# Kernel tuning notes

Hardware: AMD Instinct MI355X
Metric: run time of the kernel (lower is better)

The kernel has to match this reference:

```python
import jax, jax.numpy as jnp
import numpy as np

N_NODES = 50000


def _add_self_loops(src, dst, n):
    loop = jnp.arange(n, dtype=src.dtype)
    return jnp.concatenate([src, loop]), jnp.concatenate([dst, loop])


def gcn_conv(x, src, dst, W, b, n):
    # PyG GCNConv: out = D^-1/2 (A+I) D^-1/2 (x W) + b
    h = x @ W                                        # [N, out]
    deg = jnp.zeros((n,), h.dtype).at[dst].add(1.0)  # in-degree incl. self-loops
    dinv = jax.lax.rsqrt(jnp.maximum(deg, 1e-12))
    norm = dinv[src] * dinv[dst]                     # [E]
    msg = h[src] * norm[:, None]                     # [E, out] gather
    return jax.ops.segment_sum(msg, dst, num_segments=n) + b


def setup_inputs() -> dict:
    key = jax.random.key(0)
    ks = jax.random.split(key, 10)
    num_features, hidden = 256, 64
    x = jax.random.normal(ks[0], (N_NODES, num_features), jnp.float32)
    edge_index = jax.random.randint(ks[1], (2, 1600000), 0, N_NODES, jnp.int64)

    def glorot(k, fi, fo):
        s = jnp.sqrt(6.0 / (fi + fo)).astype(jnp.float32)
        return jax.random.uniform(k, (fi, fo), jnp.float32, -s, s)

    dims = [(num_features, 2 * hidden), (2 * hidden, hidden),
            (hidden, 2 * hidden), (2 * hidden, num_features)]
    params = {}
    for i, (fi, fo) in enumerate(dims):
        params[f"W{i+1}"] = glorot(ks[2 + i], fi, fo)
        params[f"b{i+1}"] = jnp.zeros((fo,), jnp.float32)
    return {"x": x, "edge_index": edge_index, **params}


def reference(x, edge_index, W1, b1, W2, b2, W3, b3, W4, b4):
    n = x.shape[0]
    src, dst = _add_self_loops(edge_index[0], edge_index[1], n)
    h = jax.nn.relu(gcn_conv(x, src, dst, W1, b1, n))
    z = jax.nn.relu(gcn_conv(h, src, dst, W2, b2, n))
    h = jax.nn.relu(gcn_conv(z, src, dst, W3, b3, n))
    x_hat = gcn_conv(h, src, dst, W4, b4, n)
    return x_hat
```

## Files before the change

### kernel.cpp

```cpp
#include <hip/hip_runtime.h>
#include <cstdint>
#include <cstddef>


static inline int cdiv(int a, int b) { return (a + b - 1) / b; }

typedef _Float16 half8v __attribute__((ext_vector_type(8)));
typedef float f32x4 __attribute__((ext_vector_type(4)));

#define NBMAX 784
#define SCHUNK 8192

__global__ __launch_bounds__(256) void k_bhist(const int* __restrict__ dst,
                                               int* __restrict__ bh,
                                               int E, int nb, int perBlock) {
  __shared__ int h[NBMAX];
  for (int i = threadIdx.x; i < nb; i += 256) h[i] = 0;
  __syncthreads();
  int beg = blockIdx.x * perBlock;
  int end = min(beg + perBlock, E);
  for (int e = beg + threadIdx.x; e < end; e += 256)
    atomicAdd(&h[dst[e] >> 6], 1);
  __syncthreads();
  for (int i = threadIdx.x; i < nb; i += 256)
    if (h[i]) atomicAdd(&bh[i], h[i]);
}

__global__ __launch_bounds__(256) void k_bscan(const int* __restrict__ bh,
                                               int* __restrict__ boff,
                                               int* __restrict__ bcur, int nb) {
  __shared__ int tsum[256];
  int t = threadIdx.x;
  int v[4];
  int s = 0;
#pragma unroll
  for (int i = 0; i < 4; ++i) {
    int idx = t * 4 + i;
    v[i] = (idx < nb) ? bh[idx] : 0;
    s += v[i];
  }
  tsum[t] = s;
  __syncthreads();
  int x = s;
  for (int d = 1; d < 256; d <<= 1) {
    int add = (t >= d) ? tsum[t - d] : 0;
    __syncthreads();
    x += add;
    tsum[t] = x;
    __syncthreads();
  }
  int base = x - s;
#pragma unroll
  for (int i = 0; i < 4; ++i) {
    int idx = t * 4 + i;
    if (idx < nb) { boff[idx] = base; bcur[idx] = base; }
    base += v[i];
  }
  if (t == 255) boff[nb] = base;
}

__global__ __launch_bounds__(256) void k_bscatter(const int* __restrict__ src,
                                                  const int* __restrict__ dst,
                                                  int* __restrict__ bcur,
                                                  unsigned* __restrict__ tmp,
                                                  int E, int nb) {
  __shared__ int hist[NBMAX];
  __shared__ int base[NBMAX];
  int beg = blockIdx.x * SCHUNK;
  int end = min(beg + SCHUNK, E);
  for (int i = threadIdx.x; i < nb; i += 256) hist[i] = 0;
  __syncthreads();
  for (int e = beg + threadIdx.x; e < end; e += 256)
    atomicAdd(&hist[dst[e] >> 6], 1);
  __syncthreads();
  for (int b = threadIdx.x; b < nb; b += 256) {
    int c = hist[b];
    base[b] = c ? atomicAdd(&bcur[b], c) : 0;
    hist[b] = 0;
  }
  __syncthreads();
  for (int e = beg + threadIdx.x; e < end; e += 256) {
    int d = dst[e];
    int b = d >> 6;
    int lp = atomicAdd(&hist[b], 1);
    tmp[base[b] + lp] = ((unsigned)(d & 63) << 16) | (unsigned)src[e];
  }
}

__global__ __launch_bounds__(256) void k_bsort(const unsigned* __restrict__ tmp,
                                               const int* __restrict__ boff,
                                               unsigned short* __restrict__ esrc,
                                               int* __restrict__ offs,
                                               int* __restrict__ counts,
                                               float* __restrict__ dinv,
                                               int N) {
  __shared__ int hist[64], cur[64];
  int b = blockIdx.x;
  int t = threadIdx.x;
  if (t < 64) hist[t] = 0;
  __syncthreads();
  int beg = boff[b], end = boff[b + 1];
  int cnt = end - beg;
  for (int i = t; i < cnt; i += 256) atomicAdd(&hist[tmp[beg + i] >> 16], 1);
  __syncthreads();
  if (t < 64) {
    int v = hist[t];
    int x = v;
#pragma unroll
    for (int d = 1; d < 64; d <<= 1) {
      int up = __shfl_up(x, d, 64);
      if (t >= d) x += up;
    }
    int ex = x - v;
    cur[t] = ex;
    int node = b * 64 + t;
    if (node < N) {
      counts[node] = v;
      offs[node] = beg + ex;
      dinv[node] = rsqrtf((float)(v + 1));
    }
  }
  __syncthreads();
  for (int i = t; i < cnt; i += 256) {
    unsigned v = tmp[beg + i];
    int pos = atomicAdd(&cur[v >> 16], 1);
    esrc[beg + pos] = (unsigned short)(v & 0xFFFFu);
  }
}

__global__ __launch_bounds__(256) void k_prepw(const float* __restrict__ W1,
                                               const float* __restrict__ W2,
                                               const float* __restrict__ W3,
                                               const float* __restrict__ W4,
                                               _Float16* __restrict__ W1t,
                                               _Float16* __restrict__ W2t,
                                               _Float16* __restrict__ W3t,
                                               _Float16* __restrict__ W4t,
                                               int* __restrict__ bh) {
  int t = blockIdx.x * 256 + threadIdx.x;
  if (t < NBMAX) bh[t] = 0;
  if (t < 32768) {
    int m = t >> 8, k = t & 255;
    W1t[t] = (_Float16)W1[k * 128 + m];
  } else if (t < 40960) {
    int u = t - 32768;
    int m = u >> 7, k = u & 127;
    W2t[u] = (_Float16)W2[k * 64 + m];
  } else if (t < 49152) {
    int u = t - 40960;
    int m = u >> 6, k = u & 63;
    W3t[u] = (_Float16)W3[k * 128 + m];
  } else if (t < 81920) {
    int u = t - 49152;
    int m = u >> 7, k = u & 127;
    W4t[u] = (_Float16)W4[k * 256 + m];
  }
}

template <int W, int BIAS, int RELU, int POST>
__global__ __launch_bounds__(256) void k_pull16(const _Float16* __restrict__ h,
                                                const unsigned short* __restrict__ esrc,
                                                const int* __restrict__ offs,
                                                const int* __restrict__ counts,
                                                const float* __restrict__ dinv,
                                                const float* __restrict__ bias,
                                                _Float16* __restrict__ out, int n) {
  const int LPR = W / 8;
  const int GRP = 64 / LPR;
  int node = blockIdx.x * 4 + (threadIdx.x >> 6);
  if (node >= n) return;
  int lane = threadIdx.x & 63;
  int g  = lane / LPR;
  int fl = lane % LPR;
  size_t rbase = (size_t)node * W + fl * 8;

  float acc[8] = {};
  if (g == 0) {
    half8v sv = *(const half8v*)&h[rbase];
#pragma unroll
    for (int q = 0; q < 8; ++q) acc[q] = (float)sv[q];
  }

  int beg = offs[node];
  int cnt = counts[node];
  int j = g;
  for (; j + 3 * GRP < cnt; j += 4 * GRP) {
    int s0 = esrc[beg + j];
    int s1 = esrc[beg + j + GRP];
    int s2 = esrc[beg + j + 2 * GRP];
    int s3 = esrc[beg + j + 3 * GRP];
    half8v v0 = *(const half8v*)&h[(size_t)s0 * W + fl * 8];
    half8v v1 = *(const half8v*)&h[(size_t)s1 * W + fl * 8];
    half8v v2 = *(const half8v*)&h[(size_t)s2 * W + fl * 8];
    half8v v3 = *(const half8v*)&h[(size_t)s3 * W + fl * 8];
#pragma unroll
    for (int q = 0; q < 8; ++q)
      acc[q] += ((float)v0[q] + (float)v1[q]) + ((float)v2[q] + (float)v3[q]);
  }
  for (; j < cnt; j += GRP) {
    int s = esrc[beg + j];
    half8v v = *(const half8v*)&h[(size_t)s * W + fl * 8];
#pragma unroll
    for (int q = 0; q < 8; ++q) acc[q] += (float)v[q];
  }

#pragma unroll
  for (int d = LPR; d < 64; d <<= 1) {
#pragma unroll
    for (int q = 0; q < 8; ++q) acc[q] += __shfl_xor(acc[q], d, 64);
  }

  if (g == 0) {
    float dv = dinv[node];
    float t[8];
#pragma unroll
    for (int q = 0; q < 8; ++q) t[q] = dv * acc[q];
    if (BIAS) {
#pragma unroll
      for (int q = 0; q < 8; ++q) t[q] += bias[fl * 8 + q];
    }
    if (RELU) {
#pragma unroll
      for (int q = 0; q < 8; ++q) t[q] = fmaxf(t[q], 0.f);
    }
    if (POST) {
#pragma unroll
      for (int q = 0; q < 8; ++q) t[q] *= dv;
    }
    half8v o;
#pragma unroll
    for (int q = 0; q < 8; ++q) o[q] = (_Float16)t[q];
    *(half8v*)&out[rbase] = o;
  }
}

template <int M, int K, int BIAS, int RELU, int SCALE, int AF32, int OUTF16>
__global__ __launch_bounds__(256) void k_gemm_mfma(const void* __restrict__ Av,
                                                   const _Float16* __restrict__ Wt,
                                                   const float* __restrict__ bias,
                                                   const float* __restrict__ dinv,
                                                   void* __restrict__ Cv, int N) {
  const int NT = M / 64;
  const int ST = K / 32;
  const int ROWW = K + 8;
  __shared__ _Float16 Als[64 * ROWW];

  const int tid = threadIdx.x;
  const int r0 = blockIdx.x * 64;

  const int CH = K / 8;
  for (int i = tid; i < 64 * CH; i += 256) {
    int r = i / CH, c = i % CH;
    int gr = r0 + r;
    if (gr >= N) gr = N - 1;
    half8v v;
    if (AF32) {
      const float* ap = &((const float*)Av)[(size_t)gr * K + c * 8];
      float4 f0 = *(const float4*)ap;
      float4 f1 = *(const float4*)(ap + 4);
      v[0] = (_Float16)f0.x; v[1] = (_Float16)f0.y;
      v[2] = (_Float16)f0.z; v[3] = (_Float16)f0.w;
      v[4] = (_Float16)f1.x; v[5] = (_Float16)f1.y;
      v[6] = (_Float16)f1.z; v[7] = (_Float16)f1.w;
    } else {
      v = *(const half8v*)&((const _Float16*)Av)[(size_t)gr * K + c * 8];
    }
    *(half8v*)&Als[r * ROWW + c * 8] = v;
  }

  const int w  = tid >> 6;
  const int l  = tid & 63;
  const int lr = l & 15;
  const int lk = l >> 4;

  half8v b_all[ST][NT];
#pragma unroll
  for (int s = 0; s < ST; ++s)
#pragma unroll
    for (int ct = 0; ct < NT; ++ct) {
      int col0 = (w * NT + ct) * 16;
      b_all[s][ct] = *(const half8v*)&Wt[(size_t)(col0 + lr) * K + s * 32 + lk * 8];
    }

  __syncthreads();

  for (int rt = 0; rt < 4; ++rt) {
    f32x4 acc[NT] = {};
#pragma unroll
    for (int s = 0; s < ST; ++s) {
      half8v a = *(const half8v*)&Als[(rt * 16 + lr) * ROWW + s * 32 + lk * 8];
#pragma unroll
      for (int ct = 0; ct < NT; ++ct)
        acc[ct] = __builtin_amdgcn_mfma_f32_16x16x32_f16(a, b_all[s][ct], acc[ct], 0, 0, 0);
    }

    int rbase = r0 + rt * 16;
    float dvv[4];
    int okr[4];
#pragma unroll
    for (int r = 0; r < 4; ++r) {
      int ro = rbase + lk * 4 + r;
      okr[r] = (ro < N);
      dvv[r] = (SCALE && okr[r]) ? dinv[ro] : 1.0f;
    }
#pragma unroll
    for (int ct = 0; ct < NT; ++ct) {
      int col = (w * NT + ct) * 16 + lr;
      float bs = BIAS ? bias[col] : 0.f;
#pragma unroll
      for (int r = 0; r < 4; ++r) {
        if (!okr[r]) continue;
        int ro = rbase + lk * 4 + r;
        float v = acc[ct][r] + bs;
        if (RELU) v = fmaxf(v, 0.f);
        if (SCALE) v *= dvv[r];
        if (OUTF16) ((_Float16*)Cv)[(size_t)ro * M + col] = (_Float16)v;
        else        ((float*)Cv)[(size_t)ro * M + col] = v;
      }
    }
  }
}

extern "C" void kernel_launch(void* const* d_in, const int* in_sizes, int n_in,
                              void* d_out, int out_size, void* d_ws, size_t ws_size,
                              hipStream_t stream) {
  const float* x  = (const float*)d_in[0];
  const int*   ei = (const int*)d_in[1];
  const float* W1 = (const float*)d_in[2];
  const float* b1 = (const float*)d_in[3];
  const float* W2 = (const float*)d_in[4];
  const float* b2 = (const float*)d_in[5];
  const float* W3 = (const float*)d_in[6];
  const float* b3 = (const float*)d_in[7];
  const float* W4 = (const float*)d_in[8];
  const float* b4 = (const float*)d_in[9];

  const int N = in_sizes[0] / 256;
  const int E = in_sizes[1] / 2;
  const int* src = ei;
  const int* dst = ei + E;
  const int nb = cdiv(N, 64);

  const int NP = 50176;
  int*   bh     = (int*)d_ws;
  int*   boff   = bh + NBMAX;
  int*   bcur   = boff + NBMAX;
  int*   counts = bcur + NBMAX;
  int*   offs   = counts + NP;
  float* dinv   = (float*)(offs + NP);
  unsigned short* esrc = (unsigned short*)(dinv + NP);
  _Float16* W1t = (_Float16*)(esrc + E);
  _Float16* W2t = W1t + 32768;
  _Float16* W3t = W2t + 8192;
  _Float16* W4t = W3t + 8192;
  _Float16* bufA = (_Float16*)(((uintptr_t)(W4t + 32768) + 255) & ~(uintptr_t)255);
  _Float16* bufB = bufA + (size_t)N * 128;
  _Float16* bufC = bufB + (size_t)N * 128;
  _Float16* bufD = bufC + (size_t)N * 64;
  unsigned* tmp = (unsigned*)bufA;
  float* out = (float*)d_out;

  dim3 blk(256);

  k_prepw<<<320, blk, 0, stream>>>(W1, W2, W3, W4, W1t, W2t, W3t, W4t, bh);
  {
    int nblk = 256;
    int perBlock = cdiv(E, nblk);
    k_bhist<<<nblk, blk, 0, stream>>>(dst, bh, E, nb, perBlock);
  }
  k_bscan<<<1, blk, 0, stream>>>(bh, boff, bcur, nb);
  k_bscatter<<<cdiv(E, SCHUNK), blk, 0, stream>>>(src, dst, bcur, tmp, E, nb);
  k_bsort<<<nb, blk, 0, stream>>>(tmp, boff, esrc, offs, counts, dinv, N);

  dim3 gpull(cdiv(N, 4));
  dim3 ggemm(cdiv(N, 64));

  k_gemm_mfma<128, 256, 0, 0, 1, 1, 1><<<ggemm, blk, 0, stream>>>(x, W1t, nullptr, dinv, bufA, N);
  k_pull16<128, 1, 1, 0><<<gpull, blk, 0, stream>>>(bufA, esrc, offs, counts, dinv, b1, bufB, N);
  k_gemm_mfma<64, 128, 0, 0, 1, 0, 1><<<ggemm, blk, 0, stream>>>(bufB, W2t, nullptr, dinv, bufC, N);
  k_pull16<64, 1, 1, 1><<<gpull, blk, 0, stream>>>(bufC, esrc, offs, counts, dinv, b2, bufD, N);
  k_pull16<64, 0, 0, 0><<<gpull, blk, 0, stream>>>(bufD, esrc, offs, counts, dinv, nullptr, bufC, N);
  k_gemm_mfma<128, 64, 1, 1, 1, 0, 1><<<ggemm, blk, 0, stream>>>(bufC, W3t, b3, dinv, bufA, N);
  k_pull16<128, 0, 0, 0><<<gpull, blk, 0, stream>>>(bufA, esrc, offs, counts, dinv, nullptr, bufB, N);
  k_gemm_mfma<256, 128, 1, 0, 0, 0, 0><<<ggemm, blk, 0, stream>>>(bufB, W4t, b4, nullptr, out, N);
}
```

Baseline: 287.9 us.

## Merge preprocessing kernels and overlap first GEMM with edge scatter

Weight prep and the destination histogram now run as one launch, and the bucket scan is done by whichever histogram block finishes last, detected with an atomic counter. The first GEMM no longer applies the dinv row scale, so it no longer needs degrees and runs in the same launch as the edge scatter. The first pull kernel then applies per-source dinv on the fly. Also adds a memset for the counters, a separate tmp buffer so it no longer aliases bufA, and nontemporal stores for the final fp32 output. The cost is one extra dinv gather per edge in layer 1, plus the added synchronisation logic.

```diff
diff --git a/kernel.cpp b/kernel.cpp
--- a/kernel.cpp
+++ b/kernel.cpp
@@ -10,243 +10,124 @@
 
 #define NBMAX 784
 #define SCHUNK 8192
-
-__global__ __launch_bounds__(256) void k_bhist(const int* __restrict__ dst,
-                                               int* __restrict__ bh,
-                                               int E, int nb, int perBlock) {
+#define NBH 256
+#define NPW 320
+
+__global__ __launch_bounds__(256) void k_prep_hist(
+    const float* __restrict__ W1, const float* __restrict__ W2,
+    const float* __restrict__ W3, const float* __restrict__ W4,
+    _Float16* __restrict__ W1t, _Float16* __restrict__ W2t,
+    _Float16* __restrict__ W3t, _Float16* __restrict__ W4t,
+    const int* __restrict__ dst, int* __restrict__ bh, int* __restrict__ done,
+    int* __restrict__ boff, int* __restrict__ bcur,
+    int E, int nb, int perBlock) {
+  int b = blockIdx.x;
+  int tid = threadIdx.x;
+  if (b < NPW) {
+    int t = b * 256 + tid;
+    if (t < 32768) {
+      int m = t >> 8, k = t & 255;
+      W1t[t] = (_Float16)W1[k * 128 + m];
+    } else if (t < 40960) {
+      int u = t - 32768;
+      int m = u >> 7, k = u & 127;
+      W2t[u] = (_Float16)W2[k * 64 + m];
+    } else if (t < 49152) {
+      int u = t - 40960;
+      int m = u >> 6, k = u & 63;
+      W3t[u] = (_Float16)W3[k * 128 + m];
+    } else if (t < 81920) {
+      int u = t - 49152;
+      int m = u >> 7, k = u & 127;
+      W4t[u] = (_Float16)W4[k * 256 + m];
+    }
+    return;
+  }
   __shared__ int h[NBMAX];
-  for (int i = threadIdx.x; i < nb; i += 256) h[i] = 0;
-  __syncthreads();
-  int beg = blockIdx.x * perBlock;
+  __shared__ int tsum[256];
+  __shared__ int amLast;
+  int hb = b - NPW;
+  for (int i = tid; i < nb; i += 256) h[i] = 0;
+  __syncthreads();
+  int beg = hb * perBlock;
   int end = min(beg + perBlock, E);
-  for (int e = beg + threadIdx.x; e < end; e += 256)
+  for (int e = beg + tid; e < end; e += 256)
     atomicAdd(&h[dst[e] >> 6], 1);
   __syncthreads();
-  for (int i = threadIdx.x; i < nb; i += 256)
+  for (int i = tid; i < nb; i += 256)
     if (h[i]) atomicAdd(&bh[i], h[i]);
-}
-
-__global__ __launch_bounds__(256) void k_bscan(const int* __restrict__ bh,
-                                               int* __restrict__ boff,
-                                               int* __restrict__ bcur, int nb) {
-  __shared__ int tsum[256];
-  int t = threadIdx.x;
+  __threadfence();
+  __syncthreads();
+  if (tid == 0) amLast = (atomicAdd(done, 1) == NBH - 1) ? 1 : 0;
+  __syncthreads();
+  if (!amLast) return;
   int v[4];
   int s = 0;
 #pragma unroll
   for (int i = 0; i < 4; ++i) {
-    int idx = t * 4 + i;
-    v[i] = (idx < nb) ? bh[idx] : 0;
+    int idx = tid * 4 + i;
+    v[i] = (idx < nb) ? atomicAdd(&bh[idx], 0) : 0;
     s += v[i];
   }
-  tsum[t] = s;
+  tsum[tid] = s;
   __syncthreads();
   int x = s;
   for (int d = 1; d < 256; d <<= 1) {
-    int add = (t >= d) ? tsum[t - d] : 0;
+    int add = (tid >= d) ? tsum[tid - d] : 0;
     __syncthreads();
     x += add;
-    tsum[t] = x;
+    tsum[tid] = x;
     __syncthreads();
   }
   int base = x - s;
 #pragma unroll
   for (int i = 0; i < 4; ++i) {
-    int idx = t * 4 + i;
+    int idx = tid * 4 + i;
     if (idx < nb) { boff[idx] = base; bcur[idx] = base; }
     base += v[i];
   }
-  if (t == 255) boff[nb] = base;
-}
-
-__global__ __launch_bounds__(256) void k_bscatter(const int* __restrict__ src,
-                                                  const int* __restrict__ dst,
-                                                  int* __restrict__ bcur,
-                                                  unsigned* __restrict__ tmp,
-                                                  int E, int nb) {
-  __shared__ int hist[NBMAX];
-  __shared__ int base[NBMAX];
-  int beg = blockIdx.x * SCHUNK;
+  if (tid == 255) boff[nb] = base;
+}
+
+__device__ __forceinline__ void scatter_body(int* hist, int* base,
+                                             const int* __restrict__ src,
+                                             const int* __restrict__ dst,
+                                             int* __restrict__ bcur,
+                                             unsigned* __restrict__ tmp,
+                                             int E, int nb, int b, int tid) {
+  int beg = b * SCHUNK;
   int end = min(beg + SCHUNK, E);
-  for (int i = threadIdx.x; i < nb; i += 256) hist[i] = 0;
-  __syncthreads();
-  for (int e = beg + threadIdx.x; e < end; e += 256)
+  for (int i = tid; i < nb; i += 256) hist[i] = 0;
+  __syncthreads();
+  for (int e = beg + tid; e < end; e += 256)
     atomicAdd(&hist[dst[e] >> 6], 1);
   __syncthreads();
-  for (int b = threadIdx.x; b < nb; b += 256) {
-    int c = hist[b];
-    base[b] = c ? atomicAdd(&bcur[b], c) : 0;
-    hist[b] = 0;
-  }
-  __syncthreads();
-  for (int e = beg + threadIdx.x; e < end; e += 256) {
+  for (int bb = tid; bb < nb; bb += 256) {
+    int c = hist[bb];
+    base[bb] = c ? atomicAdd(&bcur[bb], c) : 0;
+    hist[bb] = 0;
+  }
+  __syncthreads();
+  for (int e = beg + tid; e < end; e += 256) {
     int d = dst[e];
-    int b = d >> 6;
-    int lp = atomicAdd(&hist[b], 1);
-    tmp[base[b] + lp] = ((unsigned)(d & 63) << 16) | (unsigned)src[e];
-  }
-}
-
-__global__ __launch_bounds__(256) void k_bsort(const unsigned* __restrict__ tmp,
-                                               const int* __restrict__ boff,
-                                               unsigned short* __restrict__ esrc,
-                                               int* __restrict__ offs,
-                                               int* __restrict__ counts,
-                                               float* __restrict__ dinv,
-                                               int N) {
-  __shared__ int hist[64], cur[64];
-  int b = blockIdx.x;
-  int t = threadIdx.x;
-  if (t < 64) hist[t] = 0;
-  __syncthreads();
-  int beg = boff[b], end = boff[b + 1];
-  int cnt = end - beg;
-  for (int i = t; i < cnt; i += 256) atomicAdd(&hist[tmp[beg + i] >> 16], 1);
-  __syncthreads();
-  if (t < 64) {
-    int v = hist[t];
-    int x = v;
-#pragma unroll
-    for (int d = 1; d < 64; d <<= 1) {
-      int up = __shfl_up(x, d, 64);
-      if (t >= d) x += up;
-    }
-    int ex = x - v;
-    cur[t] = ex;
-    int node = b * 64 + t;
-    if (node < N) {
-      counts[node] = v;
-      offs[node] = beg + ex;
-      dinv[node] = rsqrtf((float)(v + 1));
-    }
-  }
-  __syncthreads();
-  for (int i = t; i < cnt; i += 256) {
-    unsigned v = tmp[beg + i];
-    int pos = atomicAdd(&cur[v >> 16], 1);
-    esrc[beg + pos] = (unsigned short)(v & 0xFFFFu);
-  }
-}
-
-__global__ __launch_bounds__(256) void k_prepw(const float* __restrict__ W1,
-                                               const float* __restrict__ W2,
-                                               const float* __restrict__ W3,
-                                               const float* __restrict__ W4,
-                                               _Float16* __restrict__ W1t,
-                                               _Float16* __restrict__ W2t,
-                                               _Float16* __restrict__ W3t,
-                                               _Float16* __restrict__ W4t,
-                                               int* __restrict__ bh) {
-  int t = blockIdx.x * 256 + threadIdx.x;
-  if (t < NBMAX) bh[t] = 0;
-  if (t < 32768) {
-    int m = t >> 8, k = t & 255;
-    W1t[t] = (_Float16)W1[k * 128 + m];
-  } else if (t < 40960) {
-    int u = t - 32768;
-    int m = u >> 7, k = u & 127;
-    W2t[u] = (_Float16)W2[k * 64 + m];
-  } else if (t < 49152) {
-    int u = t - 40960;
-    int m = u >> 6, k = u & 63;
-    W3t[u] = (_Float16)W3[k * 128 + m];
-  } else if (t < 81920) {
-    int u = t - 49152;
-    int m = u >> 7, k = u & 127;
-    W4t[u] = (_Float16)W4[k * 256 + m];
-  }
-}
-
-template <int W, int BIAS, int RELU, int POST>
-__global__ __launch_bounds__(256) void k_pull16(const _Float16* __restrict__ h,
-                                                const unsigned short* __restrict__ esrc,
-                                                const int* __restrict__ offs,
-                                                const int* __restrict__ counts,
-                                                const float* __restrict__ dinv,
-                                                const float* __restrict__ bias,
-                                                _Float16* __restrict__ out, int n) {
-  const int LPR = W / 8;
-  const int GRP = 64 / LPR;
-  int node = blockIdx.x * 4 + (threadIdx.x >> 6);
-  if (node >= n) return;
-  int lane = threadIdx.x & 63;
-  int g  = lane / LPR;
-  int fl = lane % LPR;
-  size_t rbase = (size_t)node * W + fl * 8;
-
-  float acc[8] = {};
-  if (g == 0) {
-    half8v sv = *(const half8v*)&h[rbase];
-#pragma unroll
-    for (int q = 0; q < 8; ++q) acc[q] = (float)sv[q];
-  }
-
-  int beg = offs[node];
-  int cnt = counts[node];
-  int j = g;
-  for (; j + 3 * GRP < cnt; j += 4 * GRP) {
-    int s0 = esrc[beg + j];
-    int s1 = esrc[beg + j + GRP];
-    int s2 = esrc[beg + j + 2 * GRP];
-    int s3 = esrc[beg + j + 3 * GRP];
-    half8v v0 = *(const half8v*)&h[(size_t)s0 * W + fl * 8];
-    half8v v1 = *(const half8v*)&h[(size_t)s1 * W + fl * 8];
-    half8v v2 = *(const half8v*)&h[(size_t)s2 * W + fl * 8];
-    half8v v3 = *(const half8v*)&h[(size_t)s3 * W + fl * 8];
-#pragma unroll
-    for (int q = 0; q < 8; ++q)
-      acc[q] += ((float)v0[q] + (float)v1[q]) + ((float)v2[q] + (float)v3[q]);
-  }
-  for (; j < cnt; j += GRP) {
-    int s = esrc[beg + j];
-    half8v v = *(const half8v*)&h[(size_t)s * W + fl * 8];
-#pragma unroll
-    for (int q = 0; q < 8; ++q) acc[q] += (float)v[q];
-  }
-
-#pragma unroll
-  for (int d = LPR; d < 64; d <<= 1) {
-#pragma unroll
-    for (int q = 0; q < 8; ++q) acc[q] += __shfl_xor(acc[q], d, 64);
-  }
-
-  if (g == 0) {
-    float dv = dinv[node];
-    float t[8];
-#pragma unroll
-    for (int q = 0; q < 8; ++q) t[q] = dv * acc[q];
-    if (BIAS) {
-#pragma unroll
-      for (int q = 0; q < 8; ++q) t[q] += bias[fl * 8 + q];
-    }
-    if (RELU) {
-#pragma unroll
-      for (int q = 0; q < 8; ++q) t[q] = fmaxf(t[q], 0.f);
-    }
-    if (POST) {
-#pragma unroll
-      for (int q = 0; q < 8; ++q) t[q] *= dv;
-    }
-    half8v o;
-#pragma unroll
-    for (int q = 0; q < 8; ++q) o[q] = (_Float16)t[q];
-    *(half8v*)&out[rbase] = o;
+    int bb = d >> 6;
+    int lp = atomicAdd(&hist[bb], 1);
+    tmp[base[bb] + lp] = ((unsigned)(d & 63) << 16) | (unsigned)src[e];
   }
 }
 
 template <int M, int K, int BIAS, int RELU, int SCALE, int AF32, int OUTF16>
-__global__ __launch_bounds__(256) void k_gemm_mfma(const void* __restrict__ Av,
-                                                   const _Float16* __restrict__ Wt,
-                                                   const float* __restrict__ bias,
-                                                   const float* __restrict__ dinv,
-                                                   void* __restrict__ Cv, int N) {
+__device__ __forceinline__ void gemm_body(_Float16* Als,
+                                          const void* __restrict__ Av,
+                                          const _Float16* __restrict__ Wt,
+                                          const float* __restrict__ bias,
+                                          const float* __restrict__ dinv,
+                                          void* __restrict__ Cv, int N,
+                                          int bx, int tid) {
   const int NT = M / 64;
   const int ST = K / 32;
   const int ROWW = K + 8;
-  __shared__ _Float16 Als[64 * ROWW];
-
-  const int tid = threadIdx.x;
-  const int r0 = blockIdx.x * 64;
+  const int r0 = bx * 64;
 
   const int CH = K / 8;
   for (int i = tid; i < 64 * CH; i += 256) {
@@ -293,7 +174,6 @@
       for (int ct = 0; ct < NT; ++ct)
         acc[ct] = __builtin_amdgcn_mfma_f32_16x16x32_f16(a, b_all[s][ct], acc[ct], 0, 0, 0);
     }
-
     int rbase = r0 + rt * 16;
     float dvv[4];
     int okr[4];
@@ -314,10 +194,172 @@
         float v = acc[ct][r] + bs;
         if (RELU) v = fmaxf(v, 0.f);
         if (SCALE) v *= dvv[r];
-        if (OUTF16) ((_Float16*)Cv)[(size_t)ro * M + col] = (_Float16)v;
-        else        ((float*)Cv)[(size_t)ro * M + col] = v;
+        if (OUTF16) {
+          ((_Float16*)Cv)[(size_t)ro * M + col] = (_Float16)v;
+        } else {
+          __builtin_nontemporal_store(v, &((float*)Cv)[(size_t)ro * M + col]);
+        }
       }
     }
+  }
+}
+
+template <int M, int K, int BIAS, int RELU, int SCALE, int AF32, int OUTF16>
+__global__ __launch_bounds__(256) void k_gemm_mfma(const void* __restrict__ Av,
+                                                   const _Float16* __restrict__ Wt,
+                                                   const float* __restrict__ bias,
+                                                   const float* __restrict__ dinv,
+                                                   void* __restrict__ Cv, int N) {
+  __shared__ __align__(16) _Float16 Als[64 * (K + 8)];
+  gemm_body<M, K, BIAS, RELU, SCALE, AF32, OUTF16>(Als, Av, Wt, bias, dinv, Cv, N,
+                                                   blockIdx.x, threadIdx.x);
+}
+
+__global__ __launch_bounds__(256) void k_scat_gemm1(const int* __restrict__ src,
+                                                    const int* __restrict__ dst,
+                                                    int* __restrict__ bcur,
+                                                    unsigned* __restrict__ tmp,
+                                                    int E, int nb, int nsb,
+                                                    const float* __restrict__ x,
+                                                    const _Float16* __restrict__ W1t,
+                                                    _Float16* __restrict__ bufA, int N) {
+  __shared__ __align__(16) _Float16 lds[64 * 264];
+  int b = blockIdx.x;
+  if (b < nsb) {
+    int* hist = (int*)lds;
+    int* base = hist + NBMAX;
+    scatter_body(hist, base, src, dst, bcur, tmp, E, nb, b, threadIdx.x);
+  } else {
+    gemm_body<128, 256, 0, 0, 0, 1, 1>(lds, x, W1t, nullptr, nullptr, bufA, N,
+                                       b - nsb, threadIdx.x);
+  }
+}
+
+__global__ __launch_bounds__(256) void k_bsort(const unsigned* __restrict__ tmp,
+                                               const int* __restrict__ boff,
+                                               unsigned short* __restrict__ esrc,
+                                               int* __restrict__ offs,
+                                               int* __restrict__ counts,
+                                               float* __restrict__ dinv,
+                                               int N) {
+  __shared__ int hist[64], cur[64];
+  int b = blockIdx.x;
+  int t = threadIdx.x;
+  if (t < 64) hist[t] = 0;
+  __syncthreads();
+  int beg = boff[b], end = boff[b + 1];
+  int cnt = end - beg;
+  for (int i = t; i < cnt; i += 256) atomicAdd(&hist[tmp[beg + i] >> 16], 1);
+  __syncthreads();
+  if (t < 64) {
+    int v = hist[t];
+    int x = v;
+#pragma unroll
+    for (int d = 1; d < 64; d <<= 1) {
+      int up = __shfl_up(x, d, 64);
+      if (t >= d) x += up;
+    }
+    int ex = x - v;
+    cur[t] = ex;
+    int node = b * 64 + t;
+    if (node < N) {
+      counts[node] = v;
+      offs[node] = beg + ex;
+      dinv[node] = rsqrtf((float)(v + 1));
+    }
+  }
+  __syncthreads();
+  for (int i = t; i < cnt; i += 256) {
+    unsigned v = tmp[beg + i];
+    int pos = atomicAdd(&cur[v >> 16], 1);
+    esrc[beg + pos] = (unsigned short)(v & 0xFFFFu);
+  }
+}
+
+template <int W, int BIAS, int RELU, int POST, int ESCALE>
+__global__ __launch_bounds__(256) void k_pull16(const _Float16* __restrict__ h,
+                                                const unsigned short* __restrict__ esrc,
+                                                const int* __restrict__ offs,
+                                                const int* __restrict__ counts,
+                                                const float* __restrict__ dinv,
+                                                const float* __restrict__ bias,
+                                                _Float16* __restrict__ out, int n) {
+  const int LPR = W / 8;
+  const int GRP = 64 / LPR;
+  int node = blockIdx.x * 4 + (threadIdx.x >> 6);
+  if (node >= n) return;
+  int lane = threadIdx.x & 63;
+  int g  = lane / LPR;
+  int fl = lane % LPR;
+  size_t rbase = (size_t)node * W + fl * 8;
+  float dvn = dinv[node];
+
+  float acc[8] = {};
+  if (g == 0) {
+    half8v sv = *(const half8v*)&h[rbase];
+    float sc = ESCALE ? dvn : 1.0f;
+#pragma unroll
+    for (int q = 0; q < 8; ++q) acc[q] = sc * (float)sv[q];
+  }
+
+  int beg = offs[node];
+  int cnt = counts[node];
+  int j = g;
+  for (; j + 3 * GRP < cnt; j += 4 * GRP) {
+    int s0 = esrc[beg + j];
+    int s1 = esrc[beg + j + GRP];
+    int s2 = esrc[beg + j + 2 * GRP];
+    int s3 = esrc[beg + j + 3 * GRP];
+    half8v v0 = *(const half8v*)&h[(size_t)s0 * W + fl * 8];
+    half8v v1 = *(const half8v*)&h[(size_t)s1 * W + fl * 8];
+    half8v v2 = *(const half8v*)&h[(size_t)s2 * W + fl * 8];
+    half8v v3 = *(const half8v*)&h[(size_t)s3 * W + fl * 8];
+    if (ESCALE) {
+      float d0 = dinv[s0], d1 = dinv[s1], d2 = dinv[s2], d3 = dinv[s3];
+#pragma unroll
+      for (int q = 0; q < 8; ++q)
+        acc[q] += (d0 * (float)v0[q] + d1 * (float)v1[q]) +
+                  (d2 * (float)v2[q] + d3 * (float)v3[q]);
+    } else {
+#pragma unroll
+      for (int q = 0; q < 8; ++q)
+        acc[q] += ((float)v0[q] + (float)v1[q]) + ((float)v2[q] + (float)v3[q]);
+    }
+  }
+  for (; j < cnt; j += GRP) {
+    int s = esrc[beg + j];
+    half8v v = *(const half8v*)&h[(size_t)s * W + fl * 8];
+    float ds = ESCALE ? dinv[s] : 1.0f;
+#pragma unroll
+    for (int q = 0; q < 8; ++q) acc[q] += ds * (float)v[q];
+  }
+
+#pragma unroll
+  for (int d = LPR; d < 64; d <<= 1) {
+#pragma unroll
+    for (int q = 0; q < 8; ++q) acc[q] += __shfl_xor(acc[q], d, 64);
+  }
+
+  if (g == 0) {
+    float t[8];
+#pragma unroll
+    for (int q = 0; q < 8; ++q) t[q] = dvn * acc[q];
+    if (BIAS) {
+#pragma unroll
+      for (int q = 0; q < 8; ++q) t[q] += bias[fl * 8 + q];
+    }
+    if (RELU) {
+#pragma unroll
+      for (int q = 0; q < 8; ++q) t[q] = fmaxf(t[q], 0.f);
+    }
+    if (POST) {
+#pragma unroll
+      for (int q = 0; q < 8; ++q) t[q] *= dvn;
+    }
+    half8v o;
+#pragma unroll
+    for (int q = 0; q < 8; ++q) o[q] = (_Float16)t[q];
+    *(half8v*)&out[rbase] = o;
   }
 }
 
@@ -340,10 +382,12 @@
   const int* src = ei;
   const int* dst = ei + E;
   const int nb = cdiv(N, 64);
+  const int nsb = cdiv(E, SCHUNK);
 
   const int NP = 50176;
   int*   bh     = (int*)d_ws;
-  int*   boff   = bh + NBMAX;
+  int*   done   = bh + NBMAX;
+  int*   boff   = bh + NBMAX + 16;
   int*   bcur   = boff + NBMAX;
   int*   counts = bcur + NBMAX;
   int*   offs   = counts + NP;
@@ -353,34 +397,32 @@
   _Float16* W2t = W1t + 32768;
   _Float16* W3t = W2t + 8192;
   _Float16* W4t = W3t + 8192;
-  _Float16* bufA = (_Float16*)(((uintptr_t)(W4t + 32768) + 255) & ~(uintptr_t)255);
+  unsigned* tmp = (unsigned*)(((uintptr_t)(W4t + 32768) + 255) & ~(uintptr_t)255);
+  _Float16* bufA = (_Float16*)(((uintptr_t)(tmp + E) + 255) & ~(uintptr_t)255);
   _Float16* bufB = bufA + (size_t)N * 128;
   _Float16* bufC = bufB + (size_t)N * 128;
   _Float16* bufD = bufC + (size_t)N * 64;
-  unsigned* tmp = (unsigned*)bufA;
   float* out = (float*)d_out;
 
   dim3 blk(256);
 
-  k_prepw<<<320, blk, 0, stream>>>(W1, W2, W3, W4, W1t, W2t, W3t, W4t, bh);
-  {
-    int nblk = 256;
-    int perBlock = cdiv(E, nblk);
-    k_bhist<<<nblk, blk, 0, stream>>>(dst, bh, E, nb, perBlock);
-  }
-  k_bscan<<<1, blk, 0, stream>>>(bh, boff, bcur, nb);
-  k_bscatter<<<cdiv(E, SCHUNK), blk, 0, stream>>>(src, dst, bcur, tmp, E, nb);
+  (void)hipMemsetAsync(bh, 0, (NBMAX + 16) * sizeof(int), stream);
+
+  k_prep_hist<<<NPW + NBH, blk, 0, stream>>>(W1, W2, W3, W4, W1t, W2t, W3t, W4t,
+                                             dst, bh, done, boff, bcur,
+                                             E, nb, cdiv(E, NBH));
+  k_scat_gemm1<<<nsb + cdiv(N, 64), blk, 0, stream>>>(src, dst, bcur, tmp, E, nb, nsb,
+                                                      x, W1t, bufA, N);
   k_bsort<<<nb, blk, 0, stream>>>(tmp, boff, esrc, offs, counts, dinv, N);
 
   dim3 gpull(cdiv(N, 4));
   dim3 ggemm(cdiv(N, 64));
 
-  k_gemm_mfma<128, 256, 0, 0, 1, 1, 1><<<ggemm, blk, 0, stream>>>(x, W1t, nullptr, dinv, bufA, N);
-  k_pull16<128, 1, 1, 0><<<gpull, blk, 0, stream>>>(bufA, esrc, offs, counts, dinv, b1, bufB, N);
+  k_pull16<128, 1, 1, 0, 1><<<gpull, blk, 0, stream>>>(bufA, esrc, offs, counts, dinv, b1, bufB, N);
   k_gemm_mfma<64, 128, 0, 0, 1, 0, 1><<<ggemm, blk, 0, stream>>>(bufB, W2t, nullptr, dinv, bufC, N);
-  k_pull16<64, 1, 1, 1><<<gpull, blk, 0, stream>>>(bufC, esrc, offs, counts, dinv, b2, bufD, N);
-  k_pull16<64, 0, 0, 0><<<gpull, blk, 0, stream>>>(bufD, esrc, offs, counts, dinv, nullptr, bufC, N);
+  k_pull16<64, 1, 1, 1, 0><<<gpull, blk, 0, stream>>>(bufC, esrc, offs, counts, dinv, b2, bufD, N);
+  k_pull16<64, 0, 0, 0, 0><<<gpull, blk, 0, stream>>>(bufD, esrc, offs, counts, dinv, nullptr, bufC, N);
   k_gemm_mfma<128, 64, 1, 1, 1, 0, 1><<<ggemm, blk, 0, stream>>>(bufC, W3t, b3, dinv, bufA, N);
-  k_pull16<128, 0, 0, 0><<<gpull, blk, 0, stream>>>(bufA, esrc, offs, counts, dinv, nullptr, bufB, N);
+  k_pull16<128, 0, 0, 0, 0><<<gpull, blk, 0, stream>>>(bufA, esrc, offs, counts, dinv, nullptr, bufB, N);
   k_gemm_mfma<256, 128, 1, 0, 0, 0, 0><<<ggemm, blk, 0, stream>>>(bufB, W4t, b4, nullptr, out, N);
 }
```

After: 288.3 us. About the same (+0.1%).
